# Performance work log

Hardware: AMD Instinct MI355X
Metric: run time of the kernel (lower is better)

Reference implementation:

```python
import jax, jax.numpy as jnp
import numpy as np

N_POINTS = 4096
DIM = 64
MAX_EDGE_LENGTH = 1e9  # large -> no MST edge is filtered, output has static shape (n-1,)


def _mst_edge_lengths(points):
    """0-dim Rips persistence death values == Euclidean MST edge lengths.

    Equivalent to gudhi RipsComplex(max_dimension=0) + flag_persistence_generators
    followed by torch.norm(input[v0] - input[v1], dim=-1). Returned sorted
    ascending (gudhi's ordering is unspecified; compare as a multiset).
    """
    n = points.shape[0]
    sq = jnp.sum(points * points, axis=1)                      # [n]
    d2 = sq[:, None] + sq[None, :] - 2.0 * (points @ points.T)  # [n,n]
    d2 = jnp.maximum(d2, 0.0)
    # safe positive diagonal so sqrt is smooth there (diagonal never selected)
    idx = jnp.arange(n)
    d2 = d2.at[idx, idx].set(1.0)
    D = jnp.sqrt(d2)                                            # [n,n] distances

    inf = jnp.asarray(jnp.inf, D.dtype)
    in_tree0 = jnp.zeros((n,), dtype=bool).at[0].set(True)
    dist0 = jnp.where(in_tree0, inf, D[0])                      # min dist to tree

    def step(carry, _):
        dist, in_tree = carry
        j = jnp.argmin(dist)            # nearest non-tree vertex
        w = dist[j]                     # MST edge length (a persistence death)
        in_tree = in_tree.at[j].set(True)
        dist = jnp.where(in_tree, inf, jnp.minimum(dist, D[j]))
        return (dist, in_tree), w

    _, lengths = jax.lax.scan(step, (dist0, in_tree0), None, length=n - 1)
    # max_edge_length filter is a no-op for MAX_EDGE_LENGTH=1e9
    return jnp.sort(lengths)


def setup_inputs() -> dict:
    key = jax.random.key(0)
    points = jax.random.normal(key, (N_POINTS, DIM), dtype=jnp.float32)
    return {"input": points}


def reference(input) -> jnp.ndarray:
    return _mst_edge_lengths(input)
```

## Files before the change

kernel.cpp:

```cpp
#include <hip/hip_runtime.h>
#include <hip/hip_bf16.h>


#define NPTS 4096
#define SENT 1e30f
#define KINF 0xFFFFFFFFFFFFFFFFull
#define INV32 0xFFFFFFFFu
#define SCAN_ROWS 2
#define SCAN_BLOCKS (NPTS / SCAN_ROWS)
#define CMAX 1024

#define HOOK_NORMAL 0
#define HOOK_FORCE_COMPACT 1

typedef short short8 __attribute__((ext_vector_type(8)));
typedef float f32x4 __attribute__((ext_vector_type(4)));

__device__ __forceinline__ float bfbits2f(unsigned int u16) {
  union { unsigned int u; float f; } c;
  c.u = u16 << 16;
  return c.f;
}

__device__ bool data_is_bf16(const unsigned short* p) {
  bool bf = true;
  for (int i = 0; i < 256; ++i) {
    float f = bfbits2f((unsigned int)p[i]);
    if (!(f > -1e6f && f < 1e6f)) bf = false;
  }
  return bf;
}

__global__ __launch_bounds__(256) void prep_kernel(
    const void* pts_raw, unsigned short* Pb, float* sq, int* comp,
    unsigned short* comp16, int* parent, unsigned long long* cheapest,
    float* edges, unsigned* cnt, unsigned* M, unsigned long long* cheapM) {
  float pf = bfbits2f((unsigned int)((const unsigned short*)pts_raw)[threadIdx.x]);
  const bool bfs = (bool)__syncthreads_and((int)(pf > -1e6f && pf < 1e6f));

  const int g = blockIdx.x * 256 + threadIdx.x;
  if (g < NPTS) {
    comp[g] = g;
    comp16[g] = (unsigned short)g;
    parent[g] = g;
    cheapest[g] = KINF;
  }
  if (g < CMAX) cheapM[g] = KINF;
  {
    uint4 mi; mi.x = INV32; mi.y = INV32; mi.z = INV32; mi.w = INV32;
    ((uint4*)M)[g] = mi;
  }
  if (g == NPTS - 1) edges[NPTS - 1] = SENT;
  if (g == 0) {
    cnt[0] = 0u;
    cnt[1] = 0u;
    cnt[2] = bfs ? 1u : 0u;
    cnt[3] = 0u;
  }

  const int row = g >> 6;
  const int lane = threadIdx.x & 63;

  unsigned short ub;
  if (bfs) {
    ub = ((const unsigned short*)pts_raw)[row * 64 + lane];
  } else {
    __hip_bfloat16 h = __float2bfloat16(((const float*)pts_raw)[row * 64 + lane]);
    ub = *(unsigned short*)&h;
  }
  Pb[row * 64 + lane] = ub;

  float v = bfbits2f((unsigned int)ub);
  float s = v * v;
#pragma unroll
  for (int m = 1; m < 64; m <<= 1) s += __shfl_xor(s, m);
  if (lane == 0) sq[row] = s;
}

__global__ __launch_bounds__(256) void dist_mfma(const unsigned short* Pb,
                                                 const float* sq,
                                                 unsigned short* Dbf,
                                                 unsigned long long* cheapest) {
  __shared__ unsigned short tile[64 * 72];

  const int t = threadIdx.x;
  const int w = t >> 6, lane = t & 63;
  const int quad = lane >> 4, l16 = lane & 15;
  const int rbase = blockIdx.y * 64 + w * 16;
  const int cbase = blockIdx.x * 64;

  const short8* Pv = (const short8*)Pb;
  short8 a0 = Pv[(rbase + l16) * 8 + quad];
  short8 a1 = Pv[(rbase + l16) * 8 + quad + 4];

  f32x4 acc[4];
#pragma unroll
  for (int c = 0; c < 4; ++c) {
    short8 b0 = Pv[(cbase + c * 16 + l16) * 8 + quad];
    short8 b1 = Pv[(cbase + c * 16 + l16) * 8 + quad + 4];
    f32x4 z = {0.f, 0.f, 0.f, 0.f};
    z = __builtin_amdgcn_mfma_f32_16x16x32_bf16(a0, b0, z, 0, 0, 0);
    z = __builtin_amdgcn_mfma_f32_16x16x32_bf16(a1, b1, z, 0, 0, 0);
    acc[c] = z;
  }

  float sr[4];
#pragma unroll
  for (int q = 0; q < 4; ++q) sr[q] = sq[rbase + quad * 4 + q];

#pragma unroll
  for (int c = 0; c < 4; ++c) {
    float sc = sq[cbase + c * 16 + l16];
#pragma unroll
    for (int q = 0; q < 4; ++q) {
      float d2 = sr[q] + sc - 2.f * acc[c][q];
      float dd = sqrtf(fmaxf(d2, 0.f));
      __hip_bfloat16 h = __float2bfloat16(dd);
      tile[(w * 16 + quad * 4 + q) * 72 + c * 16 + l16] = *(unsigned short*)&h;
    }
  }
  __syncthreads();

  for (int i = t; i < 512; i += 256) {
    int row = i >> 3, cb8 = (i & 7) * 8;
    uint4 v = *(const uint4*)&tile[row * 72 + cb8];
    *(uint4*)&Dbf[(size_t)(blockIdx.y * 64 + row) * 4096 + cbase + cb8] = v;
  }

  {
    const int r = t >> 2, cseg = (t & 3) * 16;
    const int v = blockIdx.y * 64 + r;
    const uint4* lrow = (const uint4*)&tile[r * 72 + cseg];
    uint4 v0 = lrow[0], v1 = lrow[1];
    unsigned wv[16] = {v0.x & 0xFFFFu, v0.x >> 16, v0.y & 0xFFFFu, v0.y >> 16,
                       v0.z & 0xFFFFu, v0.z >> 16, v0.w & 0xFFFFu, v0.w >> 16,
                       v1.x & 0xFFFFu, v1.x >> 16, v1.y & 0xFFFFu, v1.y >> 16,
                       v1.z & 0xFFFFu, v1.z >> 16, v1.w & 0xFFFFu, v1.w >> 16};
    unsigned long long kmin = KINF;
#pragma unroll
    for (int e = 0; e < 16; ++e) {
      const int j = cbase + cseg + e;
      if (j != v) {
        unsigned ed = (v < j) ? (((unsigned)v << 12) | (unsigned)j)
                              : (((unsigned)j << 12) | (unsigned)v);
        unsigned long long key = ((unsigned long long)wv[e] << 24) | ed;
        kmin = key < kmin ? key : kmin;
      }
    }
#pragma unroll
    for (int m = 1; m < 4; m <<= 1) {
      unsigned long long o = __shfl_xor(kmin, m);
      kmin = o < kmin ? o : kmin;
    }
    if ((t & 3) == 0) atomicMin(&cheapest[v], kmin);
  }
}

__global__ __launch_bounds__(256) void bor_scan(const unsigned short* Dbf,
                                                const unsigned short* comp16,
                                                int* parent,
                                                unsigned long long* cheapest,
                                                const unsigned* cnt) {
  if (cnt[1]) return;

  __shared__ unsigned long long redu[SCAN_ROWS][4];

  const int t = threadIdx.x;
  const int b = blockIdx.x;
  const int wave = t >> 6;
  const int gtid = b * 256 + t;
  const int vbase = b * SCAN_ROWS;

  if (gtid < NPTS) parent[gtid] = gtid;

  const uint4* c16v = (const uint4*)comp16;
  uint4 c0 = c16v[2 * t], c1 = c16v[2 * t + 1];
  unsigned mc[16] = {c0.x & 0xFFFFu, c0.x >> 16, c0.y & 0xFFFFu, c0.y >> 16,
                     c0.z & 0xFFFFu, c0.z >> 16, c0.w & 0xFFFFu, c0.w >> 16,
                     c1.x & 0xFFFFu, c1.x >> 16, c1.y & 0xFFFFu, c1.y >> 16,
                     c1.z & 0xFFFFu, c1.z >> 16, c1.w & 0xFFFFu, c1.w >> 16};

  const uint4* rp = (const uint4*)(Dbf + (size_t)vbase * NPTS);
#pragma unroll
  for (int vv = 0; vv < SCAN_ROWS; ++vv) {
    const int v = vbase + vv;
    const unsigned cv = (unsigned)comp16[v];
    uint4 a0 = rp[vv * 512 + 2 * t];
    uint4 a1 = rp[vv * 512 + 2 * t + 1];
    unsigned wv[16] = {a0.x & 0xFFFFu, a0.x >> 16, a0.y & 0xFFFFu, a0.y >> 16,
                       a0.z & 0xFFFFu, a0.z >> 16, a0.w & 0xFFFFu, a0.w >> 16,
                       a1.x & 0xFFFFu, a1.x >> 16, a1.y & 0xFFFFu, a1.y >> 16,
                       a1.z & 0xFFFFu, a1.z >> 16, a1.w & 0xFFFFu, a1.w >> 16};
    unsigned long long kmin = KINF;
#pragma unroll
    for (int e = 0; e < 16; ++e) {
      const int j = t * 16 + e;
      if (mc[e] != cv) {
        unsigned ed = (v < j) ? (((unsigned)v << 12) | (unsigned)j)
                              : (((unsigned)j << 12) | (unsigned)v);
        unsigned long long key = ((unsigned long long)wv[e] << 24) | ed;
        kmin = key < kmin ? key : kmin;
      }
    }
#pragma unroll
    for (int m = 1; m < 64; m <<= 1) {
      unsigned long long o = __shfl_xor(kmin, m);
      kmin = o < kmin ? o : kmin;
    }
    if ((t & 63) == 0) redu[vv][wave] = kmin;
  }
  __syncthreads();

  if (t < SCAN_ROWS) {
    unsigned long long k = redu[t][0];
    if (redu[t][1] < k) k = redu[t][1];
    if (redu[t][2] < k) k = redu[t][2];
    if (redu[t][3] < k) k = redu[t][3];
    if (k != KINF) atomicMin(&cheapest[(int)comp16[vbase + t]], k);
  }
}

__global__ __launch_bounds__(1024) void bor_hook(int* comp,
                                                 unsigned short* comp16,
                                                 int* parent,
                                                 unsigned long long* cheapest,
                                                 float* edges, unsigned* cnt,
                                                 int mode) {
  if (cnt[1]) return;
  const int t = threadIdx.x;

  for (int i = t; i < NPTS; i += 1024) {
    if (comp[i] == i) {
      unsigned long long key = cheapest[i];
      if (key != KINF) {
        int mx = (int)(key & 0xFFFull);
        int mn = (int)((key >> 12) & 0xFFFull);
        int ca = comp[mn], cb = comp[mx];
        int u = (ca == i) ? cb : ca;
        bool mutual = (cheapest[u] == key);
        if (!mutual || i < u) {
          unsigned pos = atomicAdd(cnt, 1u);
          edges[pos] = bfbits2f((unsigned)(key >> 24));
        }
        if (!mutual || i > u) parent[i] = u;
      }
    }
  }
  __threadfence_block();
  __syncthreads();

  for (int i = t; i < NPTS; i += 1024) {
    int r = comp[i], p;
    for (int it = 0; it < NPTS; ++it) {
      p = parent[r];
      if (p == r) break;
      r = p;
    }
    comp[i] = r;
    comp16[i] = (unsigned short)r;
    cheapest[i] = KINF;
  }
  __threadfence_block();
  __syncthreads();

  if (mode == HOOK_FORCE_COMPACT) {
    for (int i = t; i < NPTS; i += 1024)
      if (comp[i] == i) parent[i] = (int)atomicAdd(&cnt[3], 1u);
    __syncthreads();
    for (int i = t; i < NPTS; i += 1024)
      comp16[i] = (unsigned short)parent[comp[i]];
  }
  if (t == 0 && cnt[0] >= (unsigned)(NPTS - 1)) cnt[1] = 1u;
}

__global__ __launch_bounds__(256) void bor_project(const unsigned short* Dbf,
                                                   const unsigned short* comp16,
                                                   unsigned* M,
                                                   const unsigned* cnt,
                                                   unsigned long long* cheapM) {
  if (cnt[1]) return;

  __shared__ unsigned Mloc[SCAN_ROWS][CMAX];
  __shared__ unsigned long long redc[SCAN_ROWS][4];
  const int t = threadIdx.x;
  const int b = blockIdx.x;
  const int vbase = b * SCAN_ROWS;

#pragma unroll
  for (int s = 0; s < 4; ++s) {
    Mloc[0][t + 256 * s] = INV32;
    Mloc[1][t + 256 * s] = INV32;
  }
  __syncthreads();

  const uint4* c16v = (const uint4*)comp16;
  uint4 c0 = c16v[2 * t], c1 = c16v[2 * t + 1];
  unsigned mc[16] = {c0.x & 0xFFFFu, c0.x >> 16, c0.y & 0xFFFFu, c0.y >> 16,
                     c0.z & 0xFFFFu, c0.z >> 16, c0.w & 0xFFFFu, c0.w >> 16,
                     c1.x & 0xFFFFu, c1.x >> 16, c1.y & 0xFFFFu, c1.y >> 16,
                     c1.z & 0xFFFFu, c1.z >> 16, c1.w & 0xFFFFu, c1.w >> 16};

  const uint4* rp = (const uint4*)(Dbf + (size_t)vbase * NPTS);
#pragma unroll
  for (int vv = 0; vv < SCAN_ROWS; ++vv) {
    const unsigned cv = (unsigned)comp16[vbase + vv];
    uint4 a0 = rp[vv * 512 + 2 * t];
    uint4 a1 = rp[vv * 512 + 2 * t + 1];
    unsigned wv[16] = {a0.x & 0xFFFFu, a0.x >> 16, a0.y & 0xFFFFu, a0.y >> 16,
                       a0.z & 0xFFFFu, a0.z >> 16, a0.w & 0xFFFFu, a0.w >> 16,
                       a1.x & 0xFFFFu, a1.x >> 16, a1.y & 0xFFFFu, a1.y >> 16,
                       a1.z & 0xFFFFu, a1.z >> 16, a1.w & 0xFFFFu, a1.w >> 16};
#pragma unroll
    for (int e = 0; e < 16; ++e)
      if (mc[e] != cv) atomicMin(&Mloc[vv][mc[e]], wv[e]);
  }
  __syncthreads();

  const unsigned cv0 = (unsigned)comp16[vbase];
  const unsigned cv1 = (unsigned)comp16[vbase + 1];
  unsigned long long k0 = KINF, k1 = KINF;
#pragma unroll
  for (int s = 0; s < 4; ++s) {
    const unsigned col = (unsigned)(t + 256 * s);
    unsigned x = Mloc[0][col];
    if (x != INV32) {
      atomicMin(&M[cv0 * CMAX + col], x);
      unsigned lo = cv0 < col ? cv0 : col, hi = cv0 < col ? col : cv0;
      unsigned long long key =
          ((unsigned long long)x << 22) | (lo << 11) | hi;
      if (key < k0) k0 = key;
    }
    unsigned y = Mloc[1][col];
    if (y != INV32) {
      atomicMin(&M[cv1 * CMAX + col], y);
      unsigned lo = cv1 < col ? cv1 : col, hi = cv1 < col ? col : cv1;
      unsigned long long key =
          ((unsigned long long)y << 22) | (lo << 11) | hi;
      if (key < k1) k1 = key;
    }
  }

#pragma unroll
  for (int m = 1; m < 64; m <<= 1) {
    unsigned long long o0 = __shfl_xor(k0, m);
    if (o0 < k0) k0 = o0;
    unsigned long long o1 = __shfl_xor(k1, m);
    if (o1 < k1) k1 = o1;
  }
  if ((t & 63) == 0) { redc[0][t >> 6] = k0; redc[1][t >> 6] = k1; }
  __syncthreads();
  if (t < SCAN_ROWS) {
    unsigned long long k = redc[t][0];
    if (redc[t][1] < k) k = redc[t][1];
    if (redc[t][2] < k) k = redc[t][2];
    if (redc[t][3] < k) k = redc[t][3];
    if (k != KINF)
      atomicMin(&cheapM[(int)comp16[vbase + t]], k);
  }
}

__global__ __launch_bounds__(256) void mincand(const unsigned* M,
                                               const unsigned* cnt,
                                               unsigned* cand) {
  if (cnt[1]) return;
  const int C = (int)cnt[3];
  const int t = threadIdx.x;
  const int wave = t >> 6, lane = t & 63;
  const int c = blockIdx.x * 4 + wave;
  if (c >= C) return;

  unsigned best[8];
#pragma unroll
  for (int k = 0; k < 8; ++k) best[k] = INV32;
  const unsigned* Mr = M + c * CMAX;
  for (int j = lane; j < C; j += 64) {
    unsigned w = Mr[j];
    if (w == INV32) continue;
    unsigned key = (w << 10) | (unsigned)j;
    if (key < best[7]) {
      best[7] = key;
#pragma unroll
      for (int k = 7; k > 0; --k) {
        if (best[k] < best[k - 1]) {
          unsigned tmp = best[k]; best[k] = best[k - 1]; best[k - 1] = tmp;
        }
      }
    }
  }

  int head = 0;
  for (int k = 0; k < 8; ++k) {
    unsigned my = (head < 8) ? best[head] : INV32;
    unsigned long long pk = ((unsigned long long)my << 6) | (unsigned)lane;
#pragma unroll
    for (int m = 1; m < 64; m <<= 1) {
      unsigned long long o = __shfl_xor(pk, m);
      if (o < pk) pk = o;
    }
    if (lane == (int)(pk & 63u)) ++head;
    if (lane == 0) cand[c * 8 + k] = (unsigned)(pk >> 6);
  }
}

__global__ __launch_bounds__(1024) void bor_finish(const unsigned* M,
                                                   unsigned* cnt,
                                                   float* edges,
                                                   const unsigned long long* cheapM,
                                                   const unsigned* cand) {
  if (cnt[1]) return;

  __shared__ int comp2[CMAX];
  __shared__ int parent2[CMAX];
  __shared__ unsigned long long cheap2[CMAX];
  __shared__ unsigned short flaglist[CMAX];
  __shared__ int nflag;
  __shared__ int live;

  const int t = threadIdx.x;
  const int C = (int)cnt[3];
  comp2[t] = t;
  __syncthreads();

  for (int round = 0; round < 12; ++round) {
    cheap2[t] = KINF;
    if (t == 0) { live = 0; nflag = 0; }
    __syncthreads();

    if (round == 0) {
      if (t < C) cheap2[t] = cheapM[t];
    } else {
      if (t < C) {
        const int cc = comp2[t];
        bool found = false, any = false;
        const unsigned* cd = cand + t * 8;
#pragma unroll
        for (int k = 0; k < 8; ++k) {
          unsigned e = cd[k];
          if (e == INV32) break;
          any = true;
          int j = (int)(e & 1023u);
          if (comp2[j] != cc) {
            unsigned w = e >> 10;
            int lo = t < j ? t : j, hi = t < j ? j : t;
            unsigned long long key = ((unsigned long long)w << 22) |
                                     ((unsigned)lo << 11) | (unsigned)hi;
            atomicMin(&cheap2[cc], key);
            found = true;
            break;
          }
        }
        if (!found && any) {
          int idx = atomicAdd(&nflag, 1);
          flaglist[idx] = (unsigned short)t;
        }
      }
      __syncthreads();
      {
        const int wv = t >> 6, lane = t & 63;
        for (int i = wv; i < nflag; i += 16) {
          const int c = (int)flaglist[i];
          const int cc = comp2[c];
          unsigned long long kmin = KINF;
          const unsigned* Mr = M + c * CMAX;
          for (int j = lane; j < C; j += 64) {
            unsigned w = Mr[j];
            if (w != INV32 && comp2[j] != cc) {
              int lo = c < j ? c : j, hi = c < j ? j : c;
              unsigned long long key = ((unsigned long long)w << 22) |
                                       ((unsigned)lo << 11) | (unsigned)hi;
              if (key < kmin) kmin = key;
            }
          }
#pragma unroll
          for (int m = 1; m < 64; m <<= 1) {
            unsigned long long o = __shfl_xor(kmin, m);
            if (o < kmin) kmin = o;
          }
          if (lane == 0 && kmin != KINF) atomicMin(&cheap2[cc], kmin);
        }
      }
    }
    __syncthreads();

    {
      parent2[t] = t;
      if (comp2[t] == t) {
        unsigned long long key = cheap2[t];
        if (key != KINF) {
          int hi = (int)(key & 0x7FFull);
          int lo = (int)((key >> 11) & 0x7FFull);
          int ca = comp2[lo], cb = comp2[hi];
          int u = (ca == t) ? cb : ca;
          bool mutual = (cheap2[u] == key);
          if (!mutual || t < u) {
            unsigned pos = atomicAdd(cnt, 1u);
            edges[pos] = bfbits2f((unsigned)(key >> 22));
          }
          if (!mutual || t > u) parent2[t] = u;
        }
      }
    }
    __syncthreads();

    {
      int r = comp2[t], p;
      for (int it = 0; it < CMAX; ++it) {
        p = parent2[r];
        if (p == r) break;
        r = p;
      }
      comp2[t] = r;
      if (t < C && r != comp2[0]) live = 1;
    }
    __syncthreads();
    if (!live) break;
  }
}

__global__ __launch_bounds__(256) void rank_sort(const float* edges,
                                                 const unsigned* cnt,
                                                 void* out) {
  __shared__ unsigned long long wred[4][2];
  const int b = blockIdx.x;
  const int t = threadIdx.x;
  const int pbase = 4 * b;
  const float4* ev = (const float4*)edges;
  const float4 pvv = ev[b];
  const float pv0 = pvv.x, pv1 = pvv.y, pv2 = pvv.z, pv3 = pvv.w;

  int c0 = 0, c1 = 0, c2 = 0, c3 = 0;
#pragma unroll
  for (int k = 0; k < 4; ++k) {
    float4 e = ev[t + 256 * k];
    int j = 4 * (t + 256 * k);
    float va[4] = {e.x, e.y, e.z, e.w};
#pragma unroll
    for (int m = 0; m < 4; ++m) {
      const float x = va[m];
      const int xi = j + m;
      c0 += (x < pv0 || (x == pv0 && xi < pbase + 0));
      c1 += (x < pv1 || (x == pv1 && xi < pbase + 1));
      c2 += (x < pv2 || (x == pv2 && xi < pbase + 2));
      c3 += (x < pv3 || (x == pv3 && xi < pbase + 3));
    }
  }

  unsigned long long p0 = (unsigned long long)(unsigned)c0 |
                          ((unsigned long long)(unsigned)c1 << 32);
  unsigned long long p1 = (unsigned long long)(unsigned)c2 |
                          ((unsigned long long)(unsigned)c3 << 32);
#pragma unroll
  for (int m = 1; m < 64; m <<= 1) {
    p0 += __shfl_xor(p0, m);
    p1 += __shfl_xor(p1, m);
  }
  if ((t & 63) == 0) { wred[t >> 6][0] = p0; wred[t >> 6][1] = p1; }
  __syncthreads();

  if (t == 0) {
    unsigned long long a = wred[0][0] + wred[1][0] + wred[2][0] + wred[3][0];
    unsigned long long d = wred[0][1] + wred[1][1] + wred[2][1] + wred[3][1];
    const int r[4] = {(int)(a & 0xFFFFFFFFull), (int)(a >> 32),
                      (int)(d & 0xFFFFFFFFull), (int)(d >> 32)};
    const float pv[4] = {pv0, pv1, pv2, pv3};
    const bool bf = cnt[2] != 0u;
#pragma unroll
    for (int p = 0; p < 4; ++p) {
      const int pidx = pbase + p;
      if (pidx < NPTS - 1) {
        if (bf) ((__hip_bfloat16*)out)[r[p]] = __float2bfloat16(pv[p]);
        else    ((float*)out)[r[p]] = pv[p];
      }
    }
  }
}

__global__ __launch_bounds__(256) void dist_kernel(const void* pts_raw,
                                                   __hip_bfloat16* Dbf) {
  __shared__ float As[64 * 65];
  __shared__ float Bs[64 * 65];
  __shared__ float sqA[64];
  __shared__ float sqB[64];

  const int t = threadIdx.x;
  const int bx = blockIdx.x, by = blockIdx.y;
  const bool bf = data_is_bf16((const unsigned short*)pts_raw);
  const unsigned short* pu = (const unsigned short*)pts_raw;
  const float* pf = (const float*)pts_raw;

  for (int s = 0; s < 16; ++s) {
    int e = t + 256 * s;
    int r = e >> 6, c = e & 63;
    float av, bv;
    if (bf) {
      av = bfbits2f((unsigned int)pu[by * 4096 + e]);
      bv = bfbits2f((unsigned int)pu[bx * 4096 + e]);
    } else {
      av = pf[by * 4096 + e];
      bv = pf[bx * 4096 + e];
    }
    As[r * 65 + c] = av;
    Bs[r * 65 + c] = bv;
  }
  __syncthreads();

  if (t < 64) {
    float s = 0.f;
    for (int k = 0; k < 64; ++k) { float x = As[t * 65 + k]; s += x * x; }
    sqA[t] = s;
  } else if (t < 128) {
    int r = t - 64;
    float s = 0.f;
    for (int k = 0; k < 64; ++k) { float x = Bs[r * 65 + k]; s += x * x; }
    sqB[r] = s;
  }
  __syncthreads();

  const int tx = t & 15, ty = t >> 4;
  const int lr = ty * 4, lc = tx * 4;
  float acc[4][4] = {};
  for (int k = 0; k < 64; ++k) {
    float a[4], b[4];
#pragma unroll
    for (int q = 0; q < 4; ++q) a[q] = As[(lr + q) * 65 + k];
#pragma unroll
    for (int p = 0; p < 4; ++p) b[p] = Bs[(lc + p) * 65 + k];
#pragma unroll
    for (int q = 0; q < 4; ++q)
#pragma unroll
      for (int p = 0; p < 4; ++p) acc[q][p] += a[q] * b[p];
  }

#pragma unroll
  for (int q = 0; q < 4; ++q) {
    int gr = by * 64 + lr + q;
    float sa = sqA[lr + q];
#pragma unroll
    for (int p = 0; p < 4; ++p) {
      int gc = bx * 64 + lc + p;
      float d2 = sa + sqB[lc + p] - 2.f * acc[q][p];
      d2 = fmaxf(d2, 0.f);
      Dbf[(size_t)gr * 4096 + gc] = __float2bfloat16(sqrtf(d2));
    }
  }
}

__global__ __launch_bounds__(512) void prim_kernel(const unsigned short* probe,
                                                   const unsigned short* Dbf,
                                                   void* out) {
  __shared__ float len[NPTS];
  __shared__ float rv[2][8];
  __shared__ int ri[2][8];

  const int t = threadIdx.x;
  const bool bf_out = data_is_bf16(probe);

  float d[8];
  {
    const uint4* row0 = (const uint4*)(Dbf);
    uint4 v = row0[t];
    d[0] = bfbits2f(v.x & 0xffffu); d[1] = bfbits2f(v.x >> 16);
    d[2] = bfbits2f(v.y & 0xffffu); d[3] = bfbits2f(v.y >> 16);
    d[4] = bfbits2f(v.z & 0xffffu); d[5] = bfbits2f(v.z >> 16);
    d[6] = bfbits2f(v.w & 0xffffu); d[7] = bfbits2f(v.w >> 16);
    if (t == 0) d[0] = SENT;
  }

  float bv = SENT;
  int bi = 8 * t;
#pragma unroll
  for (int k = 0; k < 8; ++k)
    if (d[k] < bv) { bv = d[k]; bi = 8 * t + k; }

  for (int step = 0; step < NPTS - 1; ++step) {
    float v = bv;
    int idx = bi;
#pragma unroll
    for (int m = 1; m < 64; m <<= 1) {
      float ov = __shfl_xor(v, m);
      int oi = __shfl_xor(idx, m);
      if (ov < v) { v = ov; idx = oi; }
    }
    const int buf = step & 1;
    if ((t & 63) == 0) { rv[buf][t >> 6] = v; ri[buf][t >> 6] = idx; }
    __syncthreads();

    float w = rv[buf][0];
    int j = ri[buf][0];
#pragma unroll
    for (int u = 1; u < 8; ++u) {
      float uv = rv[buf][u];
      if (uv < w) { w = uv; j = ri[buf][u]; }
    }
    if (t == 0) len[step] = w;

    const uint4* row = (const uint4*)(Dbf + (size_t)j * NPTS);
    uint4 rw = row[t];
    float nd[8];
    nd[0] = bfbits2f(rw.x & 0xffffu); nd[1] = bfbits2f(rw.x >> 16);
    nd[2] = bfbits2f(rw.y & 0xffffu); nd[3] = bfbits2f(rw.y >> 16);
    nd[4] = bfbits2f(rw.z & 0xffffu); nd[5] = bfbits2f(rw.z >> 16);
    nd[6] = bfbits2f(rw.w & 0xffffu); nd[7] = bfbits2f(rw.w >> 16);

    bv = SENT;
    bi = 8 * t;
    const int base = 8 * t;
#pragma unroll
    for (int k = 0; k < 8; ++k) {
      float cur = d[k];
      float nn = fminf(cur, nd[k]);
      if (cur == SENT || base + k == j) nn = SENT;
      d[k] = nn;
      if (nn < bv) { bv = nn; bi = base + k; }
    }
  }

  if (t == 0) len[NPTS - 1] = SENT;
  __syncthreads();

  for (int k = 2; k <= NPTS; k <<= 1) {
    for (int jj = k >> 1; jj > 0; jj >>= 1) {
      for (int i = t; i < NPTS; i += 512) {
        int ixj = i ^ jj;
        if (ixj > i) {
          float a = len[i], b = len[ixj];
          bool up = ((i & k) == 0);
          if ((a > b) == up) { len[i] = b; len[ixj] = a; }
        }
      }
      __syncthreads();
    }
  }

  if (bf_out) {
    __hip_bfloat16* o = (__hip_bfloat16*)out;
    for (int i = t; i < NPTS - 1; i += 512) o[i] = __float2bfloat16(len[i]);
  } else {
    float* o = (float*)out;
    for (int i = t; i < NPTS - 1; i += 512) o[i] = len[i];
  }
}

extern "C" void kernel_launch(void* const* d_in, const int* in_sizes, int n_in,
                              void* d_out, int out_size, void* d_ws, size_t ws_size,
                              hipStream_t stream) {
  const void* pts = d_in[0];
  char* base = (char*)d_ws;
  __hip_bfloat16* Dbf = (__hip_bfloat16*)base;

  size_t off = 32ull << 20;
  int* comp = (int*)(base + off);                  off += (size_t)NPTS * 4;
  int* parent = (int*)(base + off);                off += (size_t)NPTS * 4;
  unsigned long long* cheapest =
      (unsigned long long*)(base + off);           off += (size_t)NPTS * 8;
  float* edges = (float*)(base + off);             off += (size_t)NPTS * 4;
  unsigned* cnt = (unsigned*)(base + off);         off += 256;
  unsigned short* Pb = (unsigned short*)(base + off); off += (size_t)NPTS * 64 * 2;
  float* sq = (float*)(base + off);                off += (size_t)NPTS * 4;
  unsigned short* comp16 = (unsigned short*)(base + off); off += (size_t)NPTS * 2;
  unsigned* M = (unsigned*)(base + off);           off += (size_t)CMAX * CMAX * 4;
  unsigned long long* cheapM =
      (unsigned long long*)(base + off);           off += (size_t)CMAX * 8;
  unsigned* cand = (unsigned*)(base + off);        off += (size_t)CMAX * 8 * 4;

  if (ws_size >= off) {
    prep_kernel<<<1024, 256, 0, stream>>>(pts, Pb, sq, comp, comp16, parent,
                                          cheapest, edges, cnt, M, cheapM);
    const unsigned short* Dus = (const unsigned short*)Dbf;
    dist_mfma<<<dim3(64, 64), 256, 0, stream>>>(Pb, sq, (unsigned short*)Dbf,
                                                cheapest);
    bor_hook<<<1, 1024, 0, stream>>>(comp, comp16, parent, cheapest, edges,
                                     cnt, HOOK_NORMAL);
    bor_scan<<<SCAN_BLOCKS, 256, 0, stream>>>(Dus, comp16, parent, cheapest,
                                              cnt);
    bor_hook<<<1, 1024, 0, stream>>>(comp, comp16, parent, cheapest, edges,
                                     cnt, HOOK_FORCE_COMPACT);
    bor_project<<<SCAN_BLOCKS, 256, 0, stream>>>(Dus, comp16, M, cnt, cheapM);
    mincand<<<CMAX / 4, 256, 0, stream>>>(M, cnt, cand);
    bor_finish<<<1, 1024, 0, stream>>>(M, cnt, edges, cheapM, cand);
    rank_sort<<<NPTS / 4, 256, 0, stream>>>(edges, cnt, d_out);
  } else {
    dist_kernel<<<dim3(64, 64), 256, 0, stream>>>(pts, Dbf);
    prim_kernel<<<1, 512, 0, stream>>>((const unsigned short*)pts,
                                       (const unsigned short*)Dbf, d_out);
  }
}
```

Before: 169.0 us.

## Replace global atomicMin component projection with per-vertex slab and per-component reduction

Result: slower. 317.6 us (+88.0%).

```diff
diff --git a/kernel.cpp b/kernel.cpp
--- a/kernel.cpp
+++ b/kernel.cpp
@@ -34,7 +34,7 @@
 __global__ __launch_bounds__(256) void prep_kernel(
     const void* pts_raw, unsigned short* Pb, float* sq, int* comp,
     unsigned short* comp16, int* parent, unsigned long long* cheapest,
-    float* edges, unsigned* cnt, unsigned* M, unsigned long long* cheapM) {
+    float* edges, unsigned* cnt) {
   float pf = bfbits2f((unsigned int)((const unsigned short*)pts_raw)[threadIdx.x]);
   const bool bfs = (bool)__syncthreads_and((int)(pf > -1e6f && pf < 1e6f));
 
@@ -44,11 +44,6 @@
     comp16[g] = (unsigned short)g;
     parent[g] = g;
     cheapest[g] = KINF;
-  }
-  if (g < CMAX) cheapM[g] = KINF;
-  {
-    uint4 mi; mi.x = INV32; mi.y = INV32; mi.z = INV32; mi.w = INV32;
-    ((uint4*)M)[g] = mi;
   }
   if (g == NPTS - 1) edges[NPTS - 1] = SENT;
   if (g == 0) {
@@ -225,9 +220,14 @@
                                                  int* parent,
                                                  unsigned long long* cheapest,
                                                  float* edges, unsigned* cnt,
-                                                 int mode) {
+                                                 int mode,
+                                                 unsigned short* vlist,
+                                                 unsigned* cstart,
+                                                 unsigned* csize) {
   if (cnt[1]) return;
   const int t = threadIdx.x;
+  __shared__ unsigned cs[CMAX];
+  __shared__ unsigned ps[CMAX];
 
   for (int i = t; i < NPTS; i += 1024) {
     if (comp[i] == i) {
@@ -269,19 +269,41 @@
     __syncthreads();
     for (int i = t; i < NPTS; i += 1024)
       comp16[i] = (unsigned short)parent[comp[i]];
+    __syncthreads();
+
+    cs[t] = 0u;
+    __syncthreads();
+    for (int i = t; i < NPTS; i += 1024) atomicAdd(&cs[comp16[i]], 1u);
+    __syncthreads();
+    ps[t] = cs[t];
+    __syncthreads();
+    for (int off = 1; off < CMAX; off <<= 1) {
+      unsigned v = (t >= off) ? ps[t - off] : 0u;
+      __syncthreads();
+      ps[t] += v;
+      __syncthreads();
+    }
+    const unsigned start = ps[t] - cs[t];
+    cstart[t] = start;
+    csize[t] = cs[t];
+    __syncthreads();
+    cs[t] = start;
+    __syncthreads();
+    for (int i = t; i < NPTS; i += 1024) {
+      unsigned slot = atomicAdd(&cs[comp16[i]], 1u);
+      vlist[slot] = (unsigned short)i;
+    }
   }
   if (t == 0 && cnt[0] >= (unsigned)(NPTS - 1)) cnt[1] = 1u;
 }
 
-__global__ __launch_bounds__(256) void bor_project(const unsigned short* Dbf,
-                                                   const unsigned short* comp16,
-                                                   unsigned* M,
-                                                   const unsigned* cnt,
-                                                   unsigned long long* cheapM) {
+__global__ __launch_bounds__(256) void project_slab(const unsigned short* Dbf,
+                                                    const unsigned short* comp16,
+                                                    uint4* slab,
+                                                    const unsigned* cnt) {
   if (cnt[1]) return;
 
   __shared__ unsigned Mloc[SCAN_ROWS][CMAX];
-  __shared__ unsigned long long redc[SCAN_ROWS][4];
   const int t = threadIdx.x;
   const int b = blockIdx.x;
   const int vbase = b * SCAN_ROWS;
@@ -316,81 +338,56 @@
   }
   __syncthreads();
 
-  const unsigned cv0 = (unsigned)comp16[vbase];
-  const unsigned cv1 = (unsigned)comp16[vbase + 1];
-  unsigned long long k0 = KINF, k1 = KINF;
-#pragma unroll
-  for (int s = 0; s < 4; ++s) {
-    const unsigned col = (unsigned)(t + 256 * s);
-    unsigned x = Mloc[0][col];
-    if (x != INV32) {
-      atomicMin(&M[cv0 * CMAX + col], x);
-      unsigned lo = cv0 < col ? cv0 : col, hi = cv0 < col ? col : cv0;
-      unsigned long long key =
-          ((unsigned long long)x << 22) | (lo << 11) | hi;
-      if (key < k0) k0 = key;
-    }
-    unsigned y = Mloc[1][col];
-    if (y != INV32) {
-      atomicMin(&M[cv1 * CMAX + col], y);
-      unsigned lo = cv1 < col ? cv1 : col, hi = cv1 < col ? col : cv1;
-      unsigned long long key =
-          ((unsigned long long)y << 22) | (lo << 11) | hi;
-      if (key < k1) k1 = key;
-    }
-  }
-
-#pragma unroll
-  for (int m = 1; m < 64; m <<= 1) {
-    unsigned long long o0 = __shfl_xor(k0, m);
-    if (o0 < k0) k0 = o0;
-    unsigned long long o1 = __shfl_xor(k1, m);
-    if (o1 < k1) k1 = o1;
-  }
-  if ((t & 63) == 0) { redc[0][t >> 6] = k0; redc[1][t >> 6] = k1; }
-  __syncthreads();
-  if (t < SCAN_ROWS) {
-    unsigned long long k = redc[t][0];
-    if (redc[t][1] < k) k = redc[t][1];
-    if (redc[t][2] < k) k = redc[t][2];
-    if (redc[t][3] < k) k = redc[t][3];
-    if (k != KINF)
-      atomicMin(&cheapM[(int)comp16[vbase + t]], k);
-  }
-}
-
-__global__ __launch_bounds__(256) void mincand(const unsigned* M,
-                                               const unsigned* cnt,
-                                               unsigned* cand) {
+#pragma unroll
+  for (int vv = 0; vv < SCAN_ROWS; ++vv) {
+    uint4 o = *(const uint4*)&Mloc[vv][4 * t];
+    slab[(unsigned)(vbase + vv) * 256u + (unsigned)t] = o;
+  }
+}
+
+__global__ __launch_bounds__(256) void project_reduce(
+    const uint4* slab, const unsigned short* vlist, const unsigned* cstart,
+    const unsigned* csize, const unsigned* cnt, unsigned* M,
+    unsigned long long* cheapM, unsigned* cand) {
   if (cnt[1]) return;
   const int C = (int)cnt[3];
+  const int c = blockIdx.x;
+  if (c >= C) return;
+
   const int t = threadIdx.x;
-  const int wave = t >> 6, lane = t & 63;
-  const int c = blockIdx.x * 4 + wave;
-  if (c >= C) return;
-
-  unsigned best[8];
-#pragma unroll
-  for (int k = 0; k < 8; ++k) best[k] = INV32;
-  const unsigned* Mr = M + c * CMAX;
-  for (int j = lane; j < C; j += 64) {
-    unsigned w = Mr[j];
-    if (w == INV32) continue;
-    unsigned key = (w << 10) | (unsigned)j;
-    if (key < best[7]) {
-      best[7] = key;
-#pragma unroll
-      for (int k = 7; k > 0; --k) {
-        if (best[k] < best[k - 1]) {
-          unsigned tmp = best[k]; best[k] = best[k - 1]; best[k - 1] = tmp;
-        }
-      }
-    }
+  const int lane = t & 63, wave = t >> 6;
+  __shared__ unsigned wc[4][8];
+
+  const unsigned base = cstart[c];
+  const unsigned n = csize[c];
+  uint4 acc;
+  acc.x = INV32; acc.y = INV32; acc.z = INV32; acc.w = INV32;
+  for (unsigned m = 0; m < n; ++m) {
+    const unsigned v = (unsigned)vlist[base + m];
+    uint4 s = slab[v * 256u + (unsigned)t];
+    acc.x = s.x < acc.x ? s.x : acc.x;
+    acc.y = s.y < acc.y ? s.y : acc.y;
+    acc.z = s.z < acc.z ? s.z : acc.z;
+    acc.w = s.w < acc.w ? s.w : acc.w;
+  }
+  ((uint4*)M)[c * 256 + t] = acc;
+
+  unsigned k4[4];
+  {
+    const unsigned col0 = 4u * (unsigned)t;
+    k4[0] = (acc.x == INV32) ? INV32 : ((acc.x << 10) | (col0 + 0u));
+    k4[1] = (acc.y == INV32) ? INV32 : ((acc.y << 10) | (col0 + 1u));
+    k4[2] = (acc.z == INV32) ? INV32 : ((acc.z << 10) | (col0 + 2u));
+    k4[3] = (acc.w == INV32) ? INV32 : ((acc.w << 10) | (col0 + 3u));
+    unsigned tmp;
+#define SW(a, b) if (k4[b] < k4[a]) { tmp = k4[a]; k4[a] = k4[b]; k4[b] = tmp; }
+    SW(0, 1) SW(2, 3) SW(0, 2) SW(1, 3) SW(1, 2)
+#undef SW
   }
 
   int head = 0;
   for (int k = 0; k < 8; ++k) {
-    unsigned my = (head < 8) ? best[head] : INV32;
+    unsigned my = (head < 4) ? k4[head] : INV32;
     unsigned long long pk = ((unsigned long long)my << 6) | (unsigned)lane;
 #pragma unroll
     for (int m = 1; m < 64; m <<= 1) {
@@ -398,7 +395,35 @@
       if (o < pk) pk = o;
     }
     if (lane == (int)(pk & 63u)) ++head;
-    if (lane == 0) cand[c * 8 + k] = (unsigned)(pk >> 6);
+    if (lane == 0) wc[wave][k] = (unsigned)(pk >> 6);
+  }
+  __syncthreads();
+
+  if (wave == 0) {
+    unsigned v = (lane < 32) ? wc[lane >> 3][lane & 7] : INV32;
+    for (int k = 0; k < 8; ++k) {
+      unsigned long long pk = ((unsigned long long)v << 6) | (unsigned)lane;
+#pragma unroll
+      for (int m = 1; m < 64; m <<= 1) {
+        unsigned long long o = __shfl_xor(pk, m);
+        if (o < pk) pk = o;
+      }
+      const unsigned e = (unsigned)(pk >> 6);
+      if (lane == (int)(pk & 63u)) v = INV32;
+      if (lane == 0) {
+        cand[c * 8 + k] = e;
+        if (k == 0) {
+          if (e == INV32) {
+            cheapM[c] = KINF;
+          } else {
+            unsigned w = e >> 10, j = e & 1023u;
+            unsigned lo = ((unsigned)c < j) ? (unsigned)c : j;
+            unsigned hi = ((unsigned)c < j) ? j : (unsigned)c;
+            cheapM[c] = ((unsigned long long)w << 22) | (lo << 11) | hi;
+          }
+        }
+      }
+    }
   }
 }
 
@@ -762,21 +787,27 @@
   unsigned long long* cheapM =
       (unsigned long long*)(base + off);           off += (size_t)CMAX * 8;
   unsigned* cand = (unsigned*)(base + off);        off += (size_t)CMAX * 8 * 4;
+  unsigned short* vlist = (unsigned short*)(base + off); off += (size_t)NPTS * 2;
+  unsigned* cstart = (unsigned*)(base + off);      off += (size_t)CMAX * 4;
+  unsigned* csize = (unsigned*)(base + off);       off += (size_t)CMAX * 4;
+  uint4* slab = (uint4*)(base + off);              off += (size_t)NPTS * CMAX * 4;
 
   if (ws_size >= off) {
     prep_kernel<<<1024, 256, 0, stream>>>(pts, Pb, sq, comp, comp16, parent,
-                                          cheapest, edges, cnt, M, cheapM);
+                                          cheapest, edges, cnt);
     const unsigned short* Dus = (const unsigned short*)Dbf;
     dist_mfma<<<dim3(64, 64), 256, 0, stream>>>(Pb, sq, (unsigned short*)Dbf,
                                                 cheapest);
     bor_hook<<<1, 1024, 0, stream>>>(comp, comp16, parent, cheapest, edges,
-                                     cnt, HOOK_NORMAL);
+                                     cnt, HOOK_NORMAL, vlist, cstart, csize);
     bor_scan<<<SCAN_BLOCKS, 256, 0, stream>>>(Dus, comp16, parent, cheapest,
                                               cnt);
     bor_hook<<<1, 1024, 0, stream>>>(comp, comp16, parent, cheapest, edges,
-                                     cnt, HOOK_FORCE_COMPACT);
-    bor_project<<<SCAN_BLOCKS, 256, 0, stream>>>(Dus, comp16, M, cnt, cheapM);
-    mincand<<<CMAX / 4, 256, 0, stream>>>(M, cnt, cand);
+                                     cnt, HOOK_FORCE_COMPACT, vlist, cstart,
+                                     csize);
+    project_slab<<<SCAN_BLOCKS, 256, 0, stream>>>(Dus, comp16, slab, cnt);
+    project_reduce<<<CMAX, 256, 0, stream>>>(slab, vlist, cstart, csize, cnt,
+                                             M, cheapM, cand);
     bor_finish<<<1, 1024, 0, stream>>>(M, cnt, edges, cheapM, cand);
     rank_sort<<<NPTS / 4, 256, 0, stream>>>(edges, cnt, d_out);
   } else {
```
